# Kernel tuning notes

Measured on AMD Instinct MI355X. Metric: run time of the kernel, lower is better.

Reference implementation:

```python
import jax, jax.numpy as jnp
import numpy as np

D_MODEL = 2048
N_HEADS = 16
HEAD_DIM = 128
ROPE_THETA = 10000.0


def _rope_cache(seq_len, dim, theta):
    inv_freq = 1.0 / (theta ** (jnp.arange(0, dim, 2, dtype=jnp.float32) / dim))
    t = jnp.arange(seq_len, dtype=jnp.float32)
    freqs = jnp.outer(t, inv_freq)          # [T, dim/2]
    emb = jnp.concatenate([freqs, freqs], axis=-1)  # [T, dim]
    return jnp.cos(emb), jnp.sin(emb)


def _rotate_half(x):
    d = x.shape[-1] // 2
    return jnp.concatenate([-x[..., d:], x[..., :d]], axis=-1)


def setup_inputs() -> dict:
    key = jax.random.key(0)
    k1, k2, k3 = jax.random.split(key, 3)
    B, T, D = 2, 2048, D_MODEL
    x = jax.random.normal(k1, (B, T, D), dtype=jnp.float32)
    w_qkv = jax.random.normal(k2, (D, 3 * D), dtype=jnp.float32) * (D ** -0.5)
    w_out = jax.random.normal(k3, (D, D), dtype=jnp.float32) * (D ** -0.5)
    return {"x": x, "w_qkv": w_qkv, "w_out": w_out}


def reference(x, w_qkv, w_out):
    B, T, D = x.shape
    H, Hd = N_HEADS, HEAD_DIM
    qkv = x @ w_qkv                                  # [B, T, 3D]
    q, k, v = jnp.split(qkv, 3, axis=-1)
    # [B, H, T, Hd]
    q = q.reshape(B, T, H, Hd).transpose(0, 2, 1, 3)
    k = k.reshape(B, T, H, Hd).transpose(0, 2, 1, 3)
    v = v.reshape(B, T, H, Hd).transpose(0, 2, 1, 3)
    cos, sin = _rope_cache(T, Hd, ROPE_THETA)        # [T, Hd]
    cos = cos[None, None]                            # [1,1,T,Hd]
    sin = sin[None, None]
    q = q * cos + _rotate_half(q) * sin
    k = k * cos + _rotate_half(k) * sin
    scale = Hd ** -0.5
    logits = jnp.einsum('bhqd,bhkd->bhqk', q, k) * scale
    causal = jnp.tril(jnp.ones((T, T), dtype=bool))
    logits = jnp.where(causal[None, None], logits, jnp.finfo(logits.dtype).min)
    attn = jax.nn.softmax(logits, axis=-1)
    out = jnp.einsum('bhqk,bhkd->bhqd', attn, v)     # [B,H,T,Hd]
    out = out.transpose(0, 2, 1, 3).reshape(B, T, D)
    return out @ w_out
```

## Files before the change

kernel.cpp:

```cpp
#include <hip/hip_runtime.h>

typedef unsigned short u16;
typedef unsigned int u32;
typedef __bf16 bf16x8 __attribute__((ext_vector_type(8)));
typedef float f32x4 __attribute__((ext_vector_type(4)));
typedef u16 u16x4 __attribute__((ext_vector_type(4)));
typedef u16 u16x8 __attribute__((ext_vector_type(8)));

#define T_SEQ 2048
#define DMODEL 2048
#define NQKV 6144
#define HD 128
#define NH 16
#define MROWS 4096

__device__ __forceinline__ u16 f2b(float f) {
  union { float f; u32 u; } a; a.f = f;
  u32 r = a.u + 0x7fffu + ((a.u >> 16) & 1u);
  return (u16)(r >> 16);
}
__device__ __forceinline__ float b2f(u16 h) {
  union { u32 u; float f; } a; a.u = ((u32)h) << 16;
  return a.f;
}
__device__ __forceinline__ void g2l16(const u16* g, u16* l) {
  __builtin_amdgcn_global_load_lds((const __attribute__((address_space(1))) u32*)g,
                                   (__attribute__((address_space(3))) u32*)l, 16, 0, 0);
}

__global__ void k_f32_to_bf16(const float* __restrict__ in, u16* __restrict__ out, int n) {
  int i = (blockIdx.x * 256 + threadIdx.x) * 8;
  if (i >= n) return;
  float4 a = *(const float4*)(in + i);
  float4 b = *(const float4*)(in + i + 4);
  u16x8 v;
  v[0] = f2b(a.x); v[1] = f2b(a.y); v[2] = f2b(a.z); v[3] = f2b(a.w);
  v[4] = f2b(b.x); v[5] = f2b(b.y); v[6] = f2b(b.z); v[7] = f2b(b.w);
  *(u16x8*)(out + i) = v;
}

__global__ void k_transpose_bf16(const float* __restrict__ in, u16* __restrict__ out,
                                 int R, int C) {
  __shared__ u16 tile[32][33];
  const int c0 = blockIdx.x * 32, r0 = blockIdx.y * 32;
  const int tx = threadIdx.x & 31, ty = threadIdx.x >> 5;
#pragma unroll
  for (int i = 0; i < 32; i += 8)
    tile[ty + i][tx] = f2b(in[(size_t)(r0 + ty + i) * C + c0 + tx]);
  __syncthreads();
#pragma unroll
  for (int i = 0; i < 32; i += 8)
    out[(size_t)(c0 + ty + i) * R + r0 + tx] = tile[tx][ty + i];
}

__global__ void k_rope_cache(float* __restrict__ csb) {
  int idx = blockIdx.x * 256 + threadIdx.x;
  int t = idx >> 6, d = idx & 63;
  float inv = powf(10000.0f, -(float)d * (1.0f / 64.0f));
  float fr = (float)t * inv;
  float2 cs = make_float2(cosf(fr), sinf(fr));
  *(float2*)(csb + (size_t)idx * 2) = cs;
}

__global__ __launch_bounds__(256, 6) void k_gemm_qkv(const u16* __restrict__ A,
                                                     const u16* __restrict__ B,
                                                     const float* __restrict__ csb,
                                                     u16* __restrict__ qr,
                                                     u16* __restrict__ kr,
                                                     u16* __restrict__ vtb) {
  __shared__ __align__(16) u16 lA[128 * 64];
  __shared__ __align__(16) u16 lB[128 * 64];
  const int K = DMODEL;
  const int tid = threadIdx.x;
  const int wid = tid >> 6, lane = tid & 63;
  const int g = lane >> 4, q = lane & 15;
  const int wr = wid >> 1, wc = wid & 1;
  const int bn = blockIdx.x, bm = blockIdx.y;
  const int l8 = lane >> 3, l7 = lane & 7;
  const f32x4 fzero = {0.f, 0.f, 0.f, 0.f};
  f32x4 acc[4][4];
#pragma unroll
  for (int m = 0; m < 4; ++m)
#pragma unroll
    for (int n = 0; n < 4; ++n) acc[m][n] = fzero;

  const u16* Ab = A + (size_t)bm * 128 * K;
  const u16* Bb = B + (size_t)bn * 128 * K;

  for (int k0 = 0; k0 < K; k0 += 64) {
    __syncthreads();
#pragma unroll
    for (int i = 0; i < 4; ++i) {
      int chunk = wid * 4 + i;
      int row = chunk * 8 + l8;
      int scol = (l7 * 8) ^ ((row & 7) << 3);
      g2l16(Ab + (size_t)row * K + k0 + scol, lA + chunk * 512);
      g2l16(Bb + (size_t)row * K + k0 + scol, lB + chunk * 512);
    }
    __syncthreads();
#pragma unroll
    for (int kk = 0; kk < 2; ++kk) {
      bf16x8 af[4], bfr[4];
#pragma unroll
      for (int m = 0; m < 4; ++m) {
        int row = wr * 64 + m * 16 + q;
        int col = (kk * 32 + g * 8) ^ ((row & 7) << 3);
        af[m] = *(const bf16x8*)(lA + row * 64 + col);
      }
#pragma unroll
      for (int n = 0; n < 4; ++n) {
        int row = wc * 32 + (n & 1) * 16 + (n >> 1) * 64 + q;
        int col = (kk * 32 + g * 8) ^ ((row & 7) << 3);
        bfr[n] = *(const bf16x8*)(lB + row * 64 + col);
      }
#pragma unroll
      for (int m = 0; m < 4; ++m)
#pragma unroll
        for (int n = 0; n < 4; ++n)
          acc[m][n] = __builtin_amdgcn_mfma_f32_16x16x32_bf16(af[m], bfr[n], acc[m][n], 0, 0, 0);
    }
  }

  const int h = bn & 15;
  const int which = bn >> 4;
  const int b = bm >> 4;
  const int bh = b * 16 + h;
  const int tb0 = (bm & 15) * 128 + wr * 64;
  const float qscale = 0.08838834764831845f;

  if (which == 2) {
    u16* vdst = vtb + (size_t)bh * HD * T_SEQ;
#pragma unroll
    for (int m = 0; m < 4; ++m)
#pragma unroll
      for (int n = 0; n < 4; ++n) {
        int c = wc * 32 + (n & 1) * 16 + (n >> 1) * 64 + q;
        int t0 = tb0 + m * 16 + g * 4;
        u16x4 pk;
#pragma unroll
        for (int r = 0; r < 4; ++r) pk[r] = f2b(acc[m][n][r]);
        *(u16x4*)(vdst + (size_t)c * T_SEQ + t0) = pk;
      }
  } else {
    u16* dst = (which ? kr : qr) + (size_t)bh * T_SEQ * HD;
    const float sc = which ? 1.0f : qscale;
#pragma unroll
    for (int m = 0; m < 4; ++m)
#pragma unroll
      for (int n = 0; n < 2; ++n) {
        int dm = wc * 32 + n * 16 + q;
#pragma unroll
        for (int r = 0; r < 4; ++r) {
          int t = tb0 + m * 16 + g * 4 + r;
          float2 cs = *(const float2*)(csb + ((size_t)t * 64 + dm) * 2);
          float x0 = acc[m][n][r];
          float x1 = acc[m][n + 2][r];
          u32 pk = (u32)f2b((x0 * cs.x - x1 * cs.y) * sc) |
                   ((u32)f2b((x1 * cs.x + x0 * cs.y) * sc) << 16);
          *(u32*)(dst + (size_t)t * HD + dm * 2) = pk;
        }
      }
  }
}

template <int EPI>
__global__ __launch_bounds__(256) void k_gemm_nt(const u16* __restrict__ A,
                                                 const u16* __restrict__ B,
                                                 void* __restrict__ Cv,
                                                 int M, int N, int K) {
  __shared__ __align__(16) u16 lA[128 * 64];
  __shared__ __align__(16) u16 lB[128 * 64];
  const int tid = threadIdx.x;
  const int wid = tid >> 6, lane = tid & 63;
  const int g = lane >> 4, q = lane & 15;
  const int wr = wid >> 1, wc = wid & 1;
  const int bn = blockIdx.x, bm = blockIdx.y;
  const int l8 = lane >> 3, l7 = lane & 7;
  const f32x4 fzero = {0.f, 0.f, 0.f, 0.f};
  f32x4 acc[4][4];
#pragma unroll
  for (int m = 0; m < 4; ++m)
#pragma unroll
    for (int n = 0; n < 4; ++n) acc[m][n] = fzero;

  const u16* Ab = A + (size_t)bm * 128 * K;
  const u16* Bb = B + (size_t)bn * 128 * K;

  for (int k0 = 0; k0 < K; k0 += 64) {
    __syncthreads();
#pragma unroll
    for (int i = 0; i < 4; ++i) {
      int chunk = wid * 4 + i;
      int row = chunk * 8 + l8;
      int scol = (l7 * 8) ^ ((row & 7) << 3);
      g2l16(Ab + (size_t)row * K + k0 + scol, lA + chunk * 512);
      g2l16(Bb + (size_t)row * K + k0 + scol, lB + chunk * 512);
    }
    __syncthreads();
#pragma unroll
    for (int kk = 0; kk < 2; ++kk) {
      bf16x8 af[4], bfr[4];
#pragma unroll
      for (int m = 0; m < 4; ++m) {
        int row = wr * 64 + m * 16 + q;
        int col = (kk * 32 + g * 8) ^ ((row & 7) << 3);
        af[m] = *(const bf16x8*)(lA + row * 64 + col);
      }
#pragma unroll
      for (int n = 0; n < 4; ++n) {
        int row = wc * 64 + n * 16 + q;
        int col = (kk * 32 + g * 8) ^ ((row & 7) << 3);
        bfr[n] = *(const bf16x8*)(lB + row * 64 + col);
      }
#pragma unroll
      for (int m = 0; m < 4; ++m)
#pragma unroll
        for (int n = 0; n < 4; ++n)
          acc[m][n] = __builtin_amdgcn_mfma_f32_16x16x32_bf16(af[m], bfr[n], acc[m][n], 0, 0, 0);
    }
  }
  const int rbase = bm * 128 + wr * 64;
  const int cbase = bn * 128 + wc * 64;
#pragma unroll
  for (int m = 0; m < 4; ++m)
#pragma unroll
    for (int n = 0; n < 4; ++n) {
      int col = cbase + n * 16 + q;
#pragma unroll
      for (int r = 0; r < 4; ++r) {
        int row = rbase + m * 16 + g * 4 + r;
        if (EPI == 0)
          ((u16*)Cv)[(size_t)row * N + col] = f2b(acc[m][n][r]);
        else
          ((float*)Cv)[(size_t)row * N + col] = acc[m][n][r];
      }
    }
}

__global__ __launch_bounds__(256) void k_attn(const u16* __restrict__ qr,
                                              const u16* __restrict__ kr,
                                              const u16* __restrict__ vtb,
                                              u16* __restrict__ ao) {
  __shared__ __align__(16) u16 lK[64 * 128];
  __shared__ __align__(16) u16 lV[128 * 64];
  __shared__ __align__(16) u16 lP[4][16 * 72];
  const int bh = blockIdx.x, b = bh >> 4, h = bh & 15;
  const int tid = threadIdx.x;
  const int wid = tid >> 6, lane = tid & 63;
  const int g = lane >> 4, q = lane & 15;
  const int l8 = lane >> 3, l7 = lane & 7;
  const u16* qb = qr + (size_t)bh * T_SEQ * HD;
  const u16* kbp = kr + (size_t)bh * T_SEQ * HD;
  const u16* vb = vtb + (size_t)bh * HD * T_SEQ;
  const f32x4 fzero = {0.f, 0.f, 0.f, 0.f};

  for (int half = 0; half < 2; ++half) {
    const int qt = half ? (int)blockIdx.y : 31 - (int)blockIdx.y;
    const int qw0 = qt * 64 + wid * 16;

    bf16x8 qf[4];
#pragma unroll
    for (int ks = 0; ks < 4; ++ks)
      qf[ks] = *(const bf16x8*)(qb + (size_t)(qw0 + q) * HD + ks * 32 + g * 8);

    f32x4 o_acc[8];
#pragma unroll
    for (int n = 0; n < 8; ++n) o_acc[n] = fzero;
    float m_run = -1e30f, l_run = 0.f;

    const int ntiles = qt + 1;
    for (int kt = 0; kt < ntiles; ++kt) {
      const int kb = kt * 64;
      __syncthreads();
#pragma unroll
      for (int i = 0; i < 4; ++i) {
        int chunk = wid * 4 + i;
        int row = chunk * 4 + g;
        int scol = (q * 8) ^ ((row & 7) << 3);
        g2l16(kbp + (size_t)(kb + row) * HD + scol, lK + chunk * 512);
      }
#pragma unroll
      for (int i = 0; i < 4; ++i) {
        int chunk = wid * 4 + i;
        int row = chunk * 8 + l8;
        int scol = (l7 * 8) ^ ((row & 7) << 3);
        g2l16(vb + (size_t)row * T_SEQ + kb + scol, lV + chunk * 512);
      }
      __syncthreads();
      {
        f32x4 st[4];
#pragma unroll
        for (int m = 0; m < 4; ++m) st[m] = fzero;
#pragma unroll
        for (int ks = 0; ks < 4; ++ks) {
#pragma unroll
          for (int m = 0; m < 4; ++m) {
            int row = m * 16 + q;
            int col = (ks * 32 + g * 8) ^ ((row & 7) << 3);
            bf16x8 kf = *(const bf16x8*)(lK + row * 128 + col);
            st[m] = __builtin_amdgcn_mfma_f32_16x16x32_bf16(kf, qf[ks], st[m], 0, 0, 0);
          }
        }
        const int qrow = qw0 + q;
        float p[4][4];
        float pmax = -1e30f;
#pragma unroll
        for (int m = 0; m < 4; ++m)
#pragma unroll
          for (int r = 0; r < 4; ++r) {
            int kcol = kb + m * 16 + g * 4 + r;
            float s = (kcol <= qrow) ? st[m][r] : -1e30f;
            p[m][r] = s;
            pmax = fmaxf(pmax, s);
          }
        pmax = fmaxf(pmax, __shfl_xor(pmax, 16));
        pmax = fmaxf(pmax, __shfl_xor(pmax, 32));
        float m_new = fmaxf(m_run, pmax);
        float corr = __expf(m_run - m_new);
        float ls = 0.f;
#pragma unroll
        for (int m = 0; m < 4; ++m)
#pragma unroll
          for (int r = 0; r < 4; ++r) {
            float e = __expf(p[m][r] - m_new);
            p[m][r] = e;
            ls += e;
          }
        ls += __shfl_xor(ls, 16);
        ls += __shfl_xor(ls, 32);
        l_run = l_run * corr + ls;
        m_run = m_new;
#pragma unroll
        for (int m = 0; m < 4; ++m) {
#pragma unroll
          for (int rp = 0; rp < 2; ++rp) {
            u32 pk = (u32)f2b(p[m][rp * 2]) | ((u32)f2b(p[m][rp * 2 + 1]) << 16);
            *(u32*)(&lP[wid][q * 72 + m * 16 + g * 4 + rp * 2]) = pk;
          }
        }
        asm volatile("s_waitcnt lgkmcnt(0)" ::: "memory");
        __builtin_amdgcn_sched_barrier(0);
        float corr4[4];
#pragma unroll
        for (int r = 0; r < 4; ++r) corr4[r] = __shfl(corr, g * 4 + r);
#pragma unroll
        for (int n = 0; n < 8; ++n) {
#pragma unroll
          for (int r = 0; r < 4; ++r) o_acc[n][r] *= corr4[r];
        }
#pragma unroll
        for (int ks = 0; ks < 2; ++ks) {
          bf16x8 pf = *(const bf16x8*)(&lP[wid][q * 72 + ks * 32 + g * 8]);
#pragma unroll
          for (int n = 0; n < 8; ++n) {
            int row = n * 16 + q;
            int col = (ks * 32 + g * 8) ^ ((row & 7) << 3);
            bf16x8 vf = *(const bf16x8*)(lV + row * 64 + col);
            o_acc[n] = __builtin_amdgcn_mfma_f32_16x16x32_bf16(pf, vf, o_acc[n], 0, 0, 0);
          }
        }
      }
    }
    float linv[4];
#pragma unroll
    for (int r = 0; r < 4; ++r) {
      float lv = __shfl(l_run, g * 4 + r);
      linv[r] = 1.0f / lv;
    }
#pragma unroll
    for (int n = 0; n < 8; ++n)
#pragma unroll
      for (int r = 0; r < 4; ++r) {
        int trow = qw0 + g * 4 + r;
        ao[(size_t)(b * T_SEQ + trow) * DMODEL + h * HD + n * 16 + q] = f2b(o_acc[n][r] * linv[r]);
      }
  }
}

extern "C" void kernel_launch(void* const* d_in, const int* in_sizes, int n_in,
                              void* d_out, int out_size, void* d_ws, size_t ws_size,
                              hipStream_t stream) {
  const float* x = (const float*)d_in[0];
  const float* w_qkv = (const float*)d_in[1];
  const float* w_out = (const float*)d_in[2];
  char* ws = (char*)d_ws;
  size_t off = 0;
  u16* xb = (u16*)(ws + off);    off += (size_t)MROWS * DMODEL * 2;
  u16* wqkvT = (u16*)(ws + off); off += (size_t)NQKV * DMODEL * 2;
  u16* woutT = (u16*)(ws + off); off += (size_t)DMODEL * DMODEL * 2;
  u16* qr = (u16*)(ws + off);    off += (size_t)32 * T_SEQ * HD * 2;
  u16* kr = (u16*)(ws + off);    off += (size_t)32 * T_SEQ * HD * 2;
  u16* vtb = (u16*)(ws + off);   off += (size_t)32 * T_SEQ * HD * 2;
  float* csb = (float*)(ws + off); off += (size_t)T_SEQ * 64 * 2 * 4;
  u16* ao = xb;

  k_f32_to_bf16<<<dim3(MROWS * DMODEL / (256 * 8)), 256, 0, stream>>>(x, xb, MROWS * DMODEL);
  k_transpose_bf16<<<dim3(NQKV / 32, DMODEL / 32), 256, 0, stream>>>(w_qkv, wqkvT, DMODEL, NQKV);
  k_transpose_bf16<<<dim3(DMODEL / 32, DMODEL / 32), 256, 0, stream>>>(w_out, woutT, DMODEL, DMODEL);
  k_rope_cache<<<dim3(T_SEQ * 64 / 256), 256, 0, stream>>>(csb);
  k_gemm_qkv<<<dim3(48, 32), 256, 0, stream>>>(xb, wqkvT, csb, qr, kr, vtb);
  k_attn<<<dim3(32, 16), 256, 0, stream>>>(qr, kr, vtb, ao);
  k_gemm_nt<1><<<dim3(DMODEL / 128, MROWS / 128), 256, 0, stream>>>(ao, woutT, d_out, MROWS, DMODEL, DMODEL);
}
```

Baseline: 269.9 us.

## Double-buffer K/V tiles in attention and skip masking on off-diagonal tiles

The attention kernel now keeps two LDS buffers for K and V. It prefetches the next tile while the current one is being computed, using one barrier per iteration instead of two. The causal mask comparison is now applied only on the final (diagonal) key tile. The QKV GEMM switches its occupancy hint to waves_per_eu(5) and adds a scheduling barrier before the epilogue. Doubling LDS use in attention may lower the number of resident blocks per CU.

Result: slower. 499.0 us (+84.9%).

```diff
diff --git a/kernel.cpp b/kernel.cpp
--- a/kernel.cpp
+++ b/kernel.cpp
@@ -62,12 +62,14 @@
   *(float2*)(csb + (size_t)idx * 2) = cs;
 }
 
-__global__ __launch_bounds__(256, 6) void k_gemm_qkv(const u16* __restrict__ A,
-                                                     const u16* __restrict__ B,
-                                                     const float* __restrict__ csb,
-                                                     u16* __restrict__ qr,
-                                                     u16* __restrict__ kr,
-                                                     u16* __restrict__ vtb) {
+__global__ __launch_bounds__(256)
+__attribute__((amdgpu_waves_per_eu(5)))
+void k_gemm_qkv(const u16* __restrict__ A,
+                const u16* __restrict__ B,
+                const float* __restrict__ csb,
+                u16* __restrict__ qr,
+                u16* __restrict__ kr,
+                u16* __restrict__ vtb) {
   __shared__ __align__(16) u16 lA[128 * 64];
   __shared__ __align__(16) u16 lB[128 * 64];
   const int K = DMODEL;
@@ -120,6 +122,7 @@
           acc[m][n] = __builtin_amdgcn_mfma_f32_16x16x32_bf16(af[m], bfr[n], acc[m][n], 0, 0, 0);
     }
   }
+  __builtin_amdgcn_sched_barrier(0);
 
   const int h = bn & 15;
   const int which = bn >> 4;
@@ -241,8 +244,8 @@
                                               const u16* __restrict__ kr,
                                               const u16* __restrict__ vtb,
                                               u16* __restrict__ ao) {
-  __shared__ __align__(16) u16 lK[64 * 128];
-  __shared__ __align__(16) u16 lV[128 * 64];
+  __shared__ __align__(16) u16 lK[2][64 * 128];
+  __shared__ __align__(16) u16 lV[2][128 * 64];
   __shared__ __align__(16) u16 lP[4][16 * 72];
   const int bh = blockIdx.x, b = bh >> 4, h = bh & 15;
   const int tid = threadIdx.x;
@@ -254,6 +257,23 @@
   const u16* vb = vtb + (size_t)bh * HD * T_SEQ;
   const f32x4 fzero = {0.f, 0.f, 0.f, 0.f};
 
+  auto stageKV = [&](int kb, int bufI) {
+#pragma unroll
+    for (int i = 0; i < 4; ++i) {
+      int chunk = wid * 4 + i;
+      int row = chunk * 4 + g;
+      int scol = (q * 8) ^ ((row & 7) << 3);
+      g2l16(kbp + (size_t)(kb + row) * HD + scol, &lK[bufI][chunk * 512]);
+    }
+#pragma unroll
+    for (int i = 0; i < 4; ++i) {
+      int chunk = wid * 4 + i;
+      int row = chunk * 8 + l8;
+      int scol = (l7 * 8) ^ ((row & 7) << 3);
+      g2l16(vb + (size_t)row * T_SEQ + kb + scol, &lV[bufI][chunk * 512]);
+    }
+  };
+
   for (int half = 0; half < 2; ++half) {
     const int qt = half ? (int)blockIdx.y : 31 - (int)blockIdx.y;
     const int qw0 = qt * 64 + wid * 16;
@@ -269,24 +289,14 @@
     float m_run = -1e30f, l_run = 0.f;
 
     const int ntiles = qt + 1;
+    stageKV(0, 0);
+    __syncthreads();
     for (int kt = 0; kt < ntiles; ++kt) {
       const int kb = kt * 64;
-      __syncthreads();
-#pragma unroll
-      for (int i = 0; i < 4; ++i) {
-        int chunk = wid * 4 + i;
-        int row = chunk * 4 + g;
-        int scol = (q * 8) ^ ((row & 7) << 3);
-        g2l16(kbp + (size_t)(kb + row) * HD + scol, lK + chunk * 512);
-      }
-#pragma unroll
-      for (int i = 0; i < 4; ++i) {
-        int chunk = wid * 4 + i;
-        int row = chunk * 8 + l8;
-        int scol = (l7 * 8) ^ ((row & 7) << 3);
-        g2l16(vb + (size_t)row * T_SEQ + kb + scol, lV + chunk * 512);
-      }
-      __syncthreads();
+      const int cb = kt & 1;
+      if (kt + 1 < ntiles) stageKV(kb + 64, cb ^ 1);
+      const u16* lKc = lK[cb];
+      const u16* lVc = lV[cb];
       {
         f32x4 st[4];
 #pragma unroll
@@ -297,22 +307,32 @@
           for (int m = 0; m < 4; ++m) {
             int row = m * 16 + q;
             int col = (ks * 32 + g * 8) ^ ((row & 7) << 3);
-            bf16x8 kf = *(const bf16x8*)(lK + row * 128 + col);
+            bf16x8 kf = *(const bf16x8*)(lKc + row * 128 + col);
             st[m] = __builtin_amdgcn_mfma_f32_16x16x32_bf16(kf, qf[ks], st[m], 0, 0, 0);
           }
         }
         const int qrow = qw0 + q;
         float p[4][4];
         float pmax = -1e30f;
-#pragma unroll
-        for (int m = 0; m < 4; ++m)
-#pragma unroll
-          for (int r = 0; r < 4; ++r) {
-            int kcol = kb + m * 16 + g * 4 + r;
-            float s = (kcol <= qrow) ? st[m][r] : -1e30f;
-            p[m][r] = s;
-            pmax = fmaxf(pmax, s);
-          }
+        if (kt == ntiles - 1) {
+#pragma unroll
+          for (int m = 0; m < 4; ++m)
+#pragma unroll
+            for (int r = 0; r < 4; ++r) {
+              int kcol = kb + m * 16 + g * 4 + r;
+              float s = (kcol <= qrow) ? st[m][r] : -1e30f;
+              p[m][r] = s;
+              pmax = fmaxf(pmax, s);
+            }
+        } else {
+#pragma unroll
+          for (int m = 0; m < 4; ++m)
+#pragma unroll
+            for (int r = 0; r < 4; ++r) {
+              p[m][r] = st[m][r];
+              pmax = fmaxf(pmax, st[m][r]);
+            }
+        }
         pmax = fmaxf(pmax, __shfl_xor(pmax, 16));
         pmax = fmaxf(pmax, __shfl_xor(pmax, 32));
         float m_new = fmaxf(m_run, pmax);
@@ -355,11 +375,12 @@
           for (int n = 0; n < 8; ++n) {
             int row = n * 16 + q;
             int col = (ks * 32 + g * 8) ^ ((row & 7) << 3);
-            bf16x8 vf = *(const bf16x8*)(lV + row * 64 + col);
+            bf16x8 vf = *(const bf16x8*)(lVc + row * 64 + col);
             o_acc[n] = __builtin_amdgcn_mfma_f32_16x16x32_bf16(pf, vf, o_acc[n], 0, 0, 0);
           }
         }
       }
+      __syncthreads();
     }
     float linv[4];
 #pragma unroll
```
